# Kernel tuning notes

Measured on AMD Instinct MI355X. Metric: run time of the kernel, lower is better.

The kernel has to match this reference:

```python
import jax, jax.numpy as jnp
import numpy as np

N_SIDE = 32          # dense voxel grid side
WINDOW = 8           # window_size
C = 512              # channels
H = 8                # num_heads
D = C // H           # head_dim = 64
EPS = 1e-12          # torch F.normalize eps


def setup_inputs() -> dict:
    key = jax.random.key(0)
    ks = jax.random.split(key, 4)
    N = N_SIDE ** 3
    g = jnp.arange(N_SIDE, dtype=jnp.int32)
    zz, yy, xx = jnp.meshgrid(g, g, g, indexing='ij')
    # coords: [N, 4] = (batch_idx, x, y, z)
    coords = jnp.stack([jnp.zeros((N,), jnp.int32),
                        xx.reshape(-1), yy.reshape(-1), zz.reshape(-1)], axis=-1)
    x_feats = jax.random.normal(ks[0], (N, C), jnp.float32)
    w_qkv = jax.random.normal(ks[1], (C, 3 * C), jnp.float32) / np.sqrt(C).astype(np.float32)
    b_qkv = jnp.zeros((3 * C,), jnp.float32)
    gamma_q = jnp.ones((H, D), jnp.float32)
    gamma_k = jnp.ones((H, D), jnp.float32)
    w_out = jax.random.normal(ks[2], (C, C), jnp.float32) / np.sqrt(C).astype(np.float32)
    b_out = jnp.zeros((C,), jnp.float32)
    return dict(x_feats=x_feats, coords=coords, w_qkv=w_qkv, b_qkv=b_qkv,
                gamma_q=gamma_q, gamma_k=gamma_k, w_out=w_out, b_out=b_out)


def _mh_rms_norm(x, gamma):
    # SparseMultiHeadRMSNorm: L2-normalize last dim, scale by gamma * sqrt(dim)
    xf = x.astype(jnp.float32)
    norm = jnp.maximum(jnp.linalg.norm(xf, axis=-1, keepdims=True), EPS)
    return ((xf / norm) * gamma * np.float32(np.sqrt(D))).astype(x.dtype)


def reference(x_feats, coords, w_qkv, b_qkv, gamma_q, gamma_k, w_out, b_out):
    N = x_feats.shape[0]
    qkv = (x_feats @ w_qkv + b_qkv).reshape(N, 3, H, D)  # [N,3,H,D]
    q = _mh_rms_norm(qkv[:, 0], gamma_q)
    k = _mh_rms_norm(qkv[:, 1], gamma_k)
    v = qkv[:, 2]
    # windowed grouping: window id from voxel coords (shift_window = (0,0,0))
    wc = coords[:, 1:] // WINDOW                       # [N,3]
    nwin = N_SIDE // WINDOW
    wid = (wc[:, 0] * nwin + wc[:, 1]) * nwin + wc[:, 2]
    order = jnp.argsort(wid, stable=True)              # gather points into windows
    inv = jnp.argsort(order)                           # scatter back
    M = WINDOW ** 3                                    # points per window (dense grid)
    W = N // M                                         # number of windows
    qg = q[order].reshape(W, M, H, D)
    kg = k[order].reshape(W, M, H, D)
    vg = v[order].reshape(W, M, H, D)
    scores = jnp.einsum('wmhd,wnhd->whmn', qg, kg) / np.float32(np.sqrt(D))
    attn = jax.nn.softmax(scores, axis=-1)
    hg = jnp.einsum('whmn,wnhd->wmhd', attn, vg)       # [W,M,H,D]
    h = hg.reshape(W * M, H * D)[inv]                  # back to original point order
    return h @ w_out + b_out
```

## Files before the change

kernel.cpp:

```cpp
#include <hip/hip_runtime.h>


typedef __attribute__((ext_vector_type(4))) float f32x4;
typedef __attribute__((ext_vector_type(8))) short s16x8;

#define MFMA(a, b, c) __builtin_amdgcn_mfma_f32_16x16x32_bf16((a), (b), (c), 0, 0, 0)

__device__ __forceinline__ short f2bf(float f) {
  union { float f; unsigned u; } v; v.f = f;
  unsigned r = v.u + 0x7fffu + ((v.u >> 16) & 1u);
  return (short)(r >> 16);
}

__device__ __forceinline__ void gload16(const void* g, void* l) {
  __builtin_amdgcn_global_load_lds(
      (const __attribute__((address_space(1))) unsigned int*)g,
      (__attribute__((address_space(3))) unsigned int*)l, 16, 0, 0);
}

__global__ __launch_bounds__(256) void transpose_w(const float* __restrict__ w,
                                                   short* __restrict__ wt,
                                                   int Ncols) {
  __shared__ float tile[64][65];
  const int t = threadIdx.x;
  const int ntn = Ncols >> 6;
  const int bk = blockIdx.x / ntn, bn = blockIdx.x % ntn;
  const int c = t & 63, r0 = t >> 6;
#pragma unroll
  for (int i = 0; i < 16; ++i) {
    int k = i * 4 + r0;
    tile[k][c] = w[(size_t)(bk * 64 + k) * Ncols + bn * 64 + c];
  }
  __syncthreads();
#pragma unroll
  for (int i = 0; i < 16; ++i) {
    int n = i * 4 + r0;
    wt[(size_t)(bn * 64 + n) * 512 + bk * 64 + c] = f2bf(tile[c][n]);
  }
}

__global__ __launch_bounds__(256) void gather_x(const float* __restrict__ x,
                                                const int* __restrict__ coords,
                                                short* __restrict__ xs,
                                                int* __restrict__ nofp) {
  const int t = threadIdx.x, lane = t & 63, wid = t >> 6;
  const int n = blockIdx.x * 4 + wid;
  const int cx = coords[n * 4 + 1], cy = coords[n * 4 + 2], cz = coords[n * 4 + 3];
  const int w = ((cx >> 3) * 4 + (cy >> 3)) * 4 + (cz >> 3);
  const int r = ((cz & 7) << 6) | ((cy & 7) << 3) | (cx & 7);
  const int p = w * 512 + r;
  const f32x4* xr = (const f32x4*)(x + (size_t)n * 512);
  f32x4 v0 = xr[lane * 2], v1 = xr[lane * 2 + 1];
  s16x8 o;
  o[0] = f2bf(v0[0]); o[1] = f2bf(v0[1]); o[2] = f2bf(v0[2]); o[3] = f2bf(v0[3]);
  o[4] = f2bf(v1[0]); o[5] = f2bf(v1[1]); o[6] = f2bf(v1[2]); o[7] = f2bf(v1[3]);
  *(s16x8*)(xs + (size_t)p * 512 + lane * 8) = o;
  if (lane == 0) nofp[p] = n;
}

__global__ __launch_bounds__(256) void gemm_qkv(
    const short* __restrict__ xs, const short* __restrict__ wt,
    const float* __restrict__ bqkv, const float* __restrict__ gq,
    const float* __restrict__ gk, short* __restrict__ Qs,
    short* __restrict__ Ks, short* __restrict__ Vt) {
  __shared__ short As[128 * 32];
  __shared__ short Bs[128 * 32];
  const int t = threadIdx.x, lane = t & 63, wid = t >> 6;
  const int bm = blockIdx.x / 12, bn = blockIdx.x % 12;
  const int wr = wid >> 1, wc = wid & 1;
  const int rowbase = bm * 128, colbase = bn * 128;
  f32x4 acc[4][4];
#pragma unroll
  for (int m = 0; m < 4; ++m)
#pragma unroll
    for (int n = 0; n < 4; ++n) acc[m][n] = (f32x4){0.f, 0.f, 0.f, 0.f};

  const int srow = lane >> 2, sslot = lane & 3;
  for (int kt = 0; kt < 16; ++kt) {
#pragma unroll
    for (int i = 0; i < 2; ++i) {
      int row = i * 64 + wid * 16 + srow;
      int gc = sslot ^ ((row >> 2) & 3);
      gload16(xs + (size_t)(rowbase + row) * 512 + kt * 32 + gc * 8,
              &As[(i * 64 + wid * 16) * 32]);
      gload16(wt + (size_t)(colbase + row) * 512 + kt * 32 + gc * 8,
              &Bs[(i * 64 + wid * 16) * 32]);
    }
    __syncthreads();
    s16x8 af[4], bfr[4];
#pragma unroll
    for (int m = 0; m < 4; ++m) {
      int row = wr * 64 + m * 16 + (lane & 15);
      int ch = (lane >> 4) ^ ((row >> 2) & 3);
      af[m] = *(const s16x8*)&As[row * 32 + ch * 8];
    }
#pragma unroll
    for (int n = 0; n < 4; ++n) {
      int row = wc * 64 + n * 16 + (lane & 15);
      int ch = (lane >> 4) ^ ((row >> 2) & 3);
      bfr[n] = *(const s16x8*)&Bs[row * 32 + ch * 8];
    }
#pragma unroll
    for (int m = 0; m < 4; ++m)
#pragma unroll
      for (int n = 0; n < 4; ++n) acc[m][n] = MFMA(af[m], bfr[n], acc[m][n]);
    __syncthreads();
  }

  const int wcb = colbase + wc * 64;
  const int which = wcb >> 9;
  const int h = (wcb >> 6) & 7;
  float bias[4], gam[4];
#pragma unroll
  for (int n = 0; n < 4; ++n) {
    int d = n * 16 + (lane & 15);
    bias[n] = bqkv[wcb + d];
    gam[n] = (which == 0) ? gq[h * 64 + d] : (which == 1) ? gk[h * 64 + d] : 1.0f;
  }
#pragma unroll
  for (int m = 0; m < 4; ++m) {
#pragma unroll
    for (int n = 0; n < 4; ++n)
#pragma unroll
      for (int j = 0; j < 4; ++j) acc[m][n][j] += bias[n];
    float scl[4] = {1.f, 1.f, 1.f, 1.f};
    if (which < 2) {
      float ss[4] = {0.f, 0.f, 0.f, 0.f};
#pragma unroll
      for (int n = 0; n < 4; ++n)
#pragma unroll
        for (int j = 0; j < 4; ++j) ss[j] += acc[m][n][j] * acc[m][n][j];
#pragma unroll
      for (int j = 0; j < 4; ++j) {
#pragma unroll
        for (int msk = 1; msk < 16; msk <<= 1) ss[j] += __shfl_xor(ss[j], msk, 64);
        float nrm = fmaxf(sqrtf(ss[j]), 1e-12f);
        scl[j] = ((which == 0) ? 1.0f : 8.0f) / nrm;
      }
    }
#pragma unroll
    for (int j = 0; j < 4; ++j) {
      int p = rowbase + wr * 64 + m * 16 + (lane >> 4) * 4 + j;
      int w = p >> 9, mm = p & 511;
#pragma unroll
      for (int n = 0; n < 4; ++n) {
        int d = n * 16 + (lane & 15);
        float v = acc[m][n][j];
        if (which == 0)
          Qs[((w * 8 + h) * 512 + mm) * 64 + d] = f2bf(v * gam[n] * scl[j]);
        else if (which == 1)
          Ks[((w * 8 + h) * 512 + mm) * 64 + d] = f2bf(v * gam[n] * scl[j]);
        else
          Vt[((w * 8 + h) * 64 + d) * 512 + mm] = f2bf(v);
      }
    }
  }
}

__global__ __launch_bounds__(256) void attn_k(const short* __restrict__ Qs,
                                              const short* __restrict__ Ks,
                                              const short* __restrict__ Vt,
                                              short* __restrict__ Hs) {
  extern __shared__ short smem[];
  short* Kl = smem;
  short* Vl = smem + 128 * 64;
  short* Pl = smem + 2 * 128 * 64;
  const int t = threadIdx.x, lane = t & 63, wid = t >> 6;
  const int qt = blockIdx.x & 3, wh = blockIdx.x >> 2;
  const short* Qb = Qs + (size_t)wh * 512 * 64;
  const short* Kb = Ks + (size_t)wh * 512 * 64;
  const short* Vb = Vt + (size_t)wh * 64 * 512;

  s16x8 aq[2][2];
#pragma unroll
  for (int m = 0; m < 2; ++m)
#pragma unroll
    for (int ks = 0; ks < 2; ++ks) {
      int row = qt * 128 + wid * 32 + m * 16 + (lane & 15);
      aq[m][ks] = *(const s16x8*)&Qb[row * 64 + ks * 32 + (lane >> 4) * 8];
    }
  f32x4 oacc[2][4];
  float rm[2][4], rl[2][4];
#pragma unroll
  for (int m = 0; m < 2; ++m) {
#pragma unroll
    for (int n = 0; n < 4; ++n) oacc[m][n] = (f32x4){0.f, 0.f, 0.f, 0.f};
#pragma unroll
    for (int j = 0; j < 4; ++j) { rm[m][j] = -1e30f; rl[m][j] = 0.f; }
  }

  for (int kt = 0; kt < 4; ++kt) {
    __syncthreads();
#pragma unroll
    for (int i = 0; i < 4; ++i) {
      int row = i * 32 + wid * 8 + (lane >> 3);
      int gc = (lane & 7) ^ (row & 7);
      gload16(Kb + (size_t)(kt * 128 + row) * 64 + gc * 8,
              &Kl[(i * 32 + wid * 8) * 64]);
    }
#pragma unroll
    for (int i = 0; i < 4; ++i) {
      int dr = i * 16 + wid * 4 + (lane >> 4);
      int gc = (lane & 15) ^ (dr & 15);
      gload16(Vb + (size_t)dr * 512 + kt * 128 + gc * 8,
              &Vl[(i * 16 + wid * 4) * 128]);
    }
    __syncthreads();

    f32x4 s[2][8];
#pragma unroll
    for (int m = 0; m < 2; ++m)
#pragma unroll
      for (int n = 0; n < 8; ++n) s[m][n] = (f32x4){0.f, 0.f, 0.f, 0.f};
#pragma unroll
    for (int ks = 0; ks < 2; ++ks)
#pragma unroll
      for (int n = 0; n < 8; ++n) {
        int kr = n * 16 + (lane & 15);
        int ch = (ks * 4 + (lane >> 4)) ^ (kr & 7);
        s16x8 bk = *(const s16x8*)&Kl[kr * 64 + ch * 8];
        s[0][n] = MFMA(aq[0][ks], bk, s[0][n]);
        s[1][n] = MFMA(aq[1][ks], bk, s[1][n]);
      }

#pragma unroll
    for (int m = 0; m < 2; ++m)
#pragma unroll
      for (int j = 0; j < 4; ++j) {
        float v = s[m][0][j];
#pragma unroll
        for (int n = 1; n < 8; ++n) v = fmaxf(v, s[m][n][j]);
#pragma unroll
        for (int msk = 1; msk < 16; msk <<= 1) v = fmaxf(v, __shfl_xor(v, msk, 64));
        float nm = fmaxf(rm[m][j], v);
        float f = __expf(rm[m][j] - nm);
        rm[m][j] = nm;
        float sum = 0.f;
#pragma unroll
        for (int n = 0; n < 8; ++n) {
          float pe = __expf(s[m][n][j] - nm);
          s[m][n][j] = pe;
          sum += pe;
        }
#pragma unroll
        for (int msk = 1; msk < 16; msk <<= 1) sum += __shfl_xor(sum, msk, 64);
        rl[m][j] = rl[m][j] * f + sum;
#pragma unroll
        for (int n2 = 0; n2 < 4; ++n2) oacc[m][n2][j] *= f;
      }

#pragma unroll
    for (int m = 0; m < 2; ++m)
#pragma unroll
      for (int n = 0; n < 8; ++n)
#pragma unroll
        for (int j = 0; j < 4; ++j) {
          int row = wid * 32 + m * 16 + (lane >> 4) * 4 + j;
          int col = n * 16 + (lane & 15);
          int ch = (col >> 3) ^ (row & 15);
          Pl[row * 128 + ch * 8 + (col & 7)] = f2bf(s[m][n][j]);
        }

#pragma unroll
    for (int ks = 0; ks < 4; ++ks) {
      s16x8 ap[2];
#pragma unroll
      for (int m = 0; m < 2; ++m) {
        int row = wid * 32 + m * 16 + (lane & 15);
        int ch = (ks * 4 + (lane >> 4)) ^ (row & 15);
        ap[m] = *(const s16x8*)&Pl[row * 128 + ch * 8];
      }
#pragma unroll
      for (int n2 = 0; n2 < 4; ++n2) {
        int dr = n2 * 16 + (lane & 15);
        int ch = (ks * 4 + (lane >> 4)) ^ (dr & 15);
        s16x8 bv = *(const s16x8*)&Vl[dr * 128 + ch * 8];
        oacc[0][n2] = MFMA(ap[0], bv, oacc[0][n2]);
        oacc[1][n2] = MFMA(ap[1], bv, oacc[1][n2]);
      }
    }
  }

  const int w = wh >> 3, hh = wh & 7;
#pragma unroll
  for (int m = 0; m < 2; ++m)
#pragma unroll
    for (int j = 0; j < 4; ++j) {
      float inv = 1.0f / rl[m][j];
      int row = qt * 128 + wid * 32 + m * 16 + (lane >> 4) * 4 + j;
      int p = w * 512 + row;
#pragma unroll
      for (int n2 = 0; n2 < 4; ++n2) {
        int d = n2 * 16 + (lane & 15);
        Hs[(size_t)p * 512 + hh * 64 + d] = f2bf(oacc[m][n2][j] * inv);
      }
    }
}

__global__ __launch_bounds__(256) void gemm_out_k(
    const short* __restrict__ Hs, const short* __restrict__ wt,
    const float* __restrict__ bout, const int* __restrict__ nofp,
    float* __restrict__ out) {
  __shared__ short As[128 * 32];
  __shared__ short Bs[128 * 32];
  const int t = threadIdx.x, lane = t & 63, wid = t >> 6;
  const int bm = blockIdx.x >> 2, bn = blockIdx.x & 3;
  const int wr = wid >> 1, wc = wid & 1;
  const int rowbase = bm * 128, colbase = bn * 128;
  f32x4 acc[4][4];
#pragma unroll
  for (int m = 0; m < 4; ++m)
#pragma unroll
    for (int n = 0; n < 4; ++n) acc[m][n] = (f32x4){0.f, 0.f, 0.f, 0.f};

  const int srow = lane >> 2, sslot = lane & 3;
  for (int kt = 0; kt < 16; ++kt) {
#pragma unroll
    for (int i = 0; i < 2; ++i) {
      int row = i * 64 + wid * 16 + srow;
      int gc = sslot ^ ((row >> 2) & 3);
      gload16(Hs + (size_t)(rowbase + row) * 512 + kt * 32 + gc * 8,
              &As[(i * 64 + wid * 16) * 32]);
      gload16(wt + (size_t)(colbase + row) * 512 + kt * 32 + gc * 8,
              &Bs[(i * 64 + wid * 16) * 32]);
    }
    __syncthreads();
    s16x8 af[4], bfr[4];
#pragma unroll
    for (int m = 0; m < 4; ++m) {
      int row = wr * 64 + m * 16 + (lane & 15);
      int ch = (lane >> 4) ^ ((row >> 2) & 3);
      af[m] = *(const s16x8*)&As[row * 32 + ch * 8];
    }
#pragma unroll
    for (int n = 0; n < 4; ++n) {
      int row = wc * 64 + n * 16 + (lane & 15);
      int ch = (lane >> 4) ^ ((row >> 2) & 3);
      bfr[n] = *(const s16x8*)&Bs[row * 32 + ch * 8];
    }
#pragma unroll
    for (int m = 0; m < 4; ++m)
#pragma unroll
      for (int n = 0; n < 4; ++n) acc[m][n] = MFMA(af[m], bfr[n], acc[m][n]);
    __syncthreads();
  }
#pragma unroll
  for (int m = 0; m < 4; ++m)
#pragma unroll
    for (int j = 0; j < 4; ++j) {
      int p = rowbase + wr * 64 + m * 16 + (lane >> 4) * 4 + j;
      int norig = nofp[p];
#pragma unroll
      for (int n = 0; n < 4; ++n) {
        int c = colbase + wc * 64 + n * 16 + (lane & 15);
        out[(size_t)norig * 512 + c] = acc[m][n][j] + bout[c];
      }
    }
}

extern "C" void kernel_launch(void* const* d_in, const int* in_sizes, int n_in,
                              void* d_out, int out_size, void* d_ws,
                              size_t ws_size, hipStream_t stream) {
  const float* x      = (const float*)d_in[0];
  const int*   coords = (const int*)d_in[1];
  const float* wqkv   = (const float*)d_in[2];
  const float* bqkv   = (const float*)d_in[3];
  const float* gq     = (const float*)d_in[4];
  const float* gk     = (const float*)d_in[5];
  const float* wout   = (const float*)d_in[6];
  const float* bout   = (const float*)d_in[7];
  float* out = (float*)d_out;
  char* ws = (char*)d_ws;

  short* xs    = (short*)(ws + 0);
  short* wqkvt = (short*)(ws + 33554432);
  short* woutt = (short*)(ws + 35127296);
  short* Qs    = (short*)(ws + 35651584);
  short* Ks    = (short*)(ws + 69206016);
  short* Vt    = (short*)(ws + 102760448);
  short* Hs    = (short*)(ws + 136314880);
  int*   nofp  = (int*)(ws + 169869312);

  transpose_w<<<dim3(192), dim3(256), 0, stream>>>(wqkv, wqkvt, 1536);
  transpose_w<<<dim3(64), dim3(256), 0, stream>>>(wout, woutt, 512);
  gather_x<<<dim3(8192), dim3(256), 0, stream>>>(x, coords, xs, nofp);
  gemm_qkv<<<dim3(3072), dim3(256), 0, stream>>>(xs, wqkvt, bqkv, gq, gk, Qs, Ks, Vt);
  attn_k<<<dim3(2048), dim3(256), 65536, stream>>>(Qs, Ks, Vt, Hs);
  gemm_out_k<<<dim3(1024), dim3(256), 0, stream>>>(Hs, woutt, bout, nofp, out);
}
```

Measured before the change: 425.2 us.

## Restructure attention into per-wave query tiles reading K/V directly from global

```diff
diff --git a/kernel.cpp b/kernel.cpp
--- a/kernel.cpp
+++ b/kernel.cpp
@@ -3,6 +3,7 @@
 
 typedef __attribute__((ext_vector_type(4))) float f32x4;
 typedef __attribute__((ext_vector_type(8))) short s16x8;
+typedef __attribute__((ext_vector_type(4))) short s16x4;
 
 #define MFMA(a, b, c) __builtin_amdgcn_mfma_f32_16x16x32_bf16((a), (b), (c), 0, 0, 0)
 
@@ -123,13 +124,13 @@
     for (int n = 0; n < 4; ++n)
 #pragma unroll
       for (int j = 0; j < 4; ++j) acc[m][n][j] += bias[n];
-    float scl[4] = {1.f, 1.f, 1.f, 1.f};
     if (which < 2) {
       float ss[4] = {0.f, 0.f, 0.f, 0.f};
 #pragma unroll
       for (int n = 0; n < 4; ++n)
 #pragma unroll
         for (int j = 0; j < 4; ++j) ss[j] += acc[m][n][j] * acc[m][n][j];
+      float scl[4];
 #pragma unroll
       for (int j = 0; j < 4; ++j) {
 #pragma unroll
@@ -137,21 +138,30 @@
         float nrm = fmaxf(sqrtf(ss[j]), 1e-12f);
         scl[j] = ((which == 0) ? 1.0f : 8.0f) / nrm;
       }
-    }
-#pragma unroll
-    for (int j = 0; j < 4; ++j) {
-      int p = rowbase + wr * 64 + m * 16 + (lane >> 4) * 4 + j;
-      int w = p >> 9, mm = p & 511;
+#pragma unroll
+      for (int j = 0; j < 4; ++j) {
+        int p = rowbase + wr * 64 + m * 16 + (lane >> 4) * 4 + j;
+        int w = p >> 9, mm = p & 511;
+#pragma unroll
+        for (int n = 0; n < 4; ++n) {
+          int d = n * 16 + (lane & 15);
+          float v = acc[m][n][j] * gam[n] * scl[j];
+          if (which == 0)
+            Qs[((w * 8 + h) * 512 + mm) * 64 + d] = f2bf(v);
+          else
+            Ks[((w * 8 + h) * 512 + mm) * 64 + d] = f2bf(v);
+        }
+      }
+    } else {
+      int pb = rowbase + wr * 64 + m * 16 + (lane >> 4) * 4;
+      int w = pb >> 9, mm = pb & 511;
 #pragma unroll
       for (int n = 0; n < 4; ++n) {
         int d = n * 16 + (lane & 15);
-        float v = acc[m][n][j];
-        if (which == 0)
-          Qs[((w * 8 + h) * 512 + mm) * 64 + d] = f2bf(v * gam[n] * scl[j]);
-        else if (which == 1)
-          Ks[((w * 8 + h) * 512 + mm) * 64 + d] = f2bf(v * gam[n] * scl[j]);
-        else
-          Vt[((w * 8 + h) * 64 + d) * 512 + mm] = f2bf(v);
+        s16x4 pk;
+#pragma unroll
+        for (int j = 0; j < 4; ++j) pk[j] = f2bf(acc[m][n][j]);
+        *(s16x4*)&Vt[((size_t)(w * 8 + h) * 64 + d) * 512 + mm] = pk;
       }
     }
   }
@@ -161,120 +171,106 @@
                                               const short* __restrict__ Ks,
                                               const short* __restrict__ Vt,
                                               short* __restrict__ Hs) {
-  extern __shared__ short smem[];
-  short* Kl = smem;
-  short* Vl = smem + 128 * 64;
-  short* Pl = smem + 2 * 128 * 64;
+  __shared__ short Pl[4][32 * 64];
   const int t = threadIdx.x, lane = t & 63, wid = t >> 6;
-  const int qt = blockIdx.x & 3, wh = blockIdx.x >> 2;
+  const int bid = blockIdx.x;
+  const int swz = (bid & 7) * 256 + (bid >> 3);
+  const int wv = swz * 4 + wid;
+  const int wh = wv >> 4;
+  const int qt = wv & 15;
   const short* Qb = Qs + (size_t)wh * 512 * 64;
   const short* Kb = Ks + (size_t)wh * 512 * 64;
   const short* Vb = Vt + (size_t)wh * 64 * 512;
+  short* slab = Pl[wid];
 
   s16x8 aq[2][2];
 #pragma unroll
-  for (int m = 0; m < 2; ++m)
+  for (int mi = 0; mi < 2; ++mi)
 #pragma unroll
     for (int ks = 0; ks < 2; ++ks) {
-      int row = qt * 128 + wid * 32 + m * 16 + (lane & 15);
-      aq[m][ks] = *(const s16x8*)&Qb[row * 64 + ks * 32 + (lane >> 4) * 8];
+      int row = qt * 32 + mi * 16 + (lane & 15);
+      aq[mi][ks] = *(const s16x8*)&Qb[row * 64 + ks * 32 + (lane >> 4) * 8];
     }
   f32x4 oacc[2][4];
   float rm[2][4], rl[2][4];
 #pragma unroll
-  for (int m = 0; m < 2; ++m) {
-#pragma unroll
-    for (int n = 0; n < 4; ++n) oacc[m][n] = (f32x4){0.f, 0.f, 0.f, 0.f};
-#pragma unroll
-    for (int j = 0; j < 4; ++j) { rm[m][j] = -1e30f; rl[m][j] = 0.f; }
-  }
-
-  for (int kt = 0; kt < 4; ++kt) {
-    __syncthreads();
-#pragma unroll
-    for (int i = 0; i < 4; ++i) {
-      int row = i * 32 + wid * 8 + (lane >> 3);
-      int gc = (lane & 7) ^ (row & 7);
-      gload16(Kb + (size_t)(kt * 128 + row) * 64 + gc * 8,
-              &Kl[(i * 32 + wid * 8) * 64]);
-    }
-#pragma unroll
-    for (int i = 0; i < 4; ++i) {
-      int dr = i * 16 + wid * 4 + (lane >> 4);
-      int gc = (lane & 15) ^ (dr & 15);
-      gload16(Vb + (size_t)dr * 512 + kt * 128 + gc * 8,
-              &Vl[(i * 16 + wid * 4) * 128]);
-    }
-    __syncthreads();
-
-    f32x4 s[2][8];
-#pragma unroll
-    for (int m = 0; m < 2; ++m)
-#pragma unroll
-      for (int n = 0; n < 8; ++n) s[m][n] = (f32x4){0.f, 0.f, 0.f, 0.f};
+  for (int mi = 0; mi < 2; ++mi) {
+#pragma unroll
+    for (int n = 0; n < 4; ++n) oacc[mi][n] = (f32x4){0.f, 0.f, 0.f, 0.f};
+#pragma unroll
+    for (int j = 0; j < 4; ++j) { rm[mi][j] = -1e30f; rl[mi][j] = 0.f; }
+  }
+
+  for (int kt = 0; kt < 8; ++kt) {
+    const int kb = kt * 64;
+    f32x4 s[2][4];
+#pragma unroll
+    for (int mi = 0; mi < 2; ++mi)
+#pragma unroll
+      for (int n = 0; n < 4; ++n) s[mi][n] = (f32x4){0.f, 0.f, 0.f, 0.f};
 #pragma unroll
     for (int ks = 0; ks < 2; ++ks)
 #pragma unroll
-      for (int n = 0; n < 8; ++n) {
-        int kr = n * 16 + (lane & 15);
-        int ch = (ks * 4 + (lane >> 4)) ^ (kr & 7);
-        s16x8 bk = *(const s16x8*)&Kl[kr * 64 + ch * 8];
+      for (int n = 0; n < 4; ++n) {
+        int kr = kb + n * 16 + (lane & 15);
+        s16x8 bk = *(const s16x8*)&Kb[kr * 64 + ks * 32 + (lane >> 4) * 8];
         s[0][n] = MFMA(aq[0][ks], bk, s[0][n]);
         s[1][n] = MFMA(aq[1][ks], bk, s[1][n]);
       }
 
 #pragma unroll
-    for (int m = 0; m < 2; ++m)
+    for (int mi = 0; mi < 2; ++mi)
 #pragma unroll
       for (int j = 0; j < 4; ++j) {
-        float v = s[m][0][j];
-#pragma unroll
-        for (int n = 1; n < 8; ++n) v = fmaxf(v, s[m][n][j]);
+        float v = fmaxf(fmaxf(s[mi][0][j], s[mi][1][j]),
+                        fmaxf(s[mi][2][j], s[mi][3][j]));
 #pragma unroll
         for (int msk = 1; msk < 16; msk <<= 1) v = fmaxf(v, __shfl_xor(v, msk, 64));
-        float nm = fmaxf(rm[m][j], v);
-        float f = __expf(rm[m][j] - nm);
-        rm[m][j] = nm;
+        if (!__all(v - rm[mi][j] <= 8.0f)) {
+          float nm = fmaxf(rm[mi][j], v);
+          float f = __expf(rm[mi][j] - nm);
+          rm[mi][j] = nm;
+          rl[mi][j] *= f;
+#pragma unroll
+          for (int n2 = 0; n2 < 4; ++n2) oacc[mi][n2][j] *= f;
+        }
         float sum = 0.f;
 #pragma unroll
-        for (int n = 0; n < 8; ++n) {
-          float pe = __expf(s[m][n][j] - nm);
-          s[m][n][j] = pe;
+        for (int n = 0; n < 4; ++n) {
+          float pe = __expf(s[mi][n][j] - rm[mi][j]);
+          s[mi][n][j] = pe;
           sum += pe;
         }
 #pragma unroll
         for (int msk = 1; msk < 16; msk <<= 1) sum += __shfl_xor(sum, msk, 64);
-        rl[m][j] = rl[m][j] * f + sum;
-#pragma unroll
-        for (int n2 = 0; n2 < 4; ++n2) oacc[m][n2][j] *= f;
-      }
-
-#pragma unroll
-    for (int m = 0; m < 2; ++m)
-#pragma unroll
-      for (int n = 0; n < 8; ++n)
+        rl[mi][j] += sum;
+      }
+
+#pragma unroll
+    for (int mi = 0; mi < 2; ++mi)
+#pragma unroll
+      for (int n = 0; n < 4; ++n)
 #pragma unroll
         for (int j = 0; j < 4; ++j) {
-          int row = wid * 32 + m * 16 + (lane >> 4) * 4 + j;
+          int r = mi * 16 + (lane >> 4) * 4 + j;
           int col = n * 16 + (lane & 15);
-          int ch = (col >> 3) ^ (row & 15);
-          Pl[row * 128 + ch * 8 + (col & 7)] = f2bf(s[m][n][j]);
+          slab[r * 64 + (((col >> 3) ^ (r & 7)) << 3) + (col & 7)] =
+              f2bf(s[mi][n][j]);
         }
 
 #pragma unroll
-    for (int ks = 0; ks < 4; ++ks) {
+    for (int ks = 0; ks < 2; ++ks) {
       s16x8 ap[2];
 #pragma unroll
-      for (int m = 0; m < 2; ++m) {
-        int row = wid * 32 + m * 16 + (lane & 15);
-        int ch = (ks * 4 + (lane >> 4)) ^ (row & 15);
-        ap[m] = *(const s16x8*)&Pl[row * 128 + ch * 8];
+      for (int mi = 0; mi < 2; ++mi) {
+        int row = mi * 16 + (lane & 15);
+        int ch = (ks * 4 + (lane >> 4)) ^ (row & 7);
+        ap[mi] = *(const s16x8*)&slab[row * 64 + ch * 8];
       }
 #pragma unroll
       for (int n2 = 0; n2 < 4; ++n2) {
         int dr = n2 * 16 + (lane & 15);
-        int ch = (ks * 4 + (lane >> 4)) ^ (dr & 15);
-        s16x8 bv = *(const s16x8*)&Vl[dr * 128 + ch * 8];
+        s16x8 bv = *(const s16x8*)&Vb[dr * 512 + kb + ks * 32 + (lane >> 4) * 8];
         oacc[0][n2] = MFMA(ap[0], bv, oacc[0][n2]);
         oacc[1][n2] = MFMA(ap[1], bv, oacc[1][n2]);
       }
@@ -283,16 +279,16 @@
 
   const int w = wh >> 3, hh = wh & 7;
 #pragma unroll
-  for (int m = 0; m < 2; ++m)
+  for (int mi = 0; mi < 2; ++mi)
 #pragma unroll
     for (int j = 0; j < 4; ++j) {
-      float inv = 1.0f / rl[m][j];
-      int row = qt * 128 + wid * 32 + m * 16 + (lane >> 4) * 4 + j;
+      float inv = 1.0f / rl[mi][j];
+      int row = qt * 32 + mi * 16 + (lane >> 4) * 4 + j;
       int p = w * 512 + row;
 #pragma unroll
       for (int n2 = 0; n2 < 4; ++n2) {
         int d = n2 * 16 + (lane & 15);
-        Hs[(size_t)p * 512 + hh * 64 + d] = f2bf(oacc[m][n2][j] * inv);
+        Hs[(size_t)p * 512 + hh * 64 + d] = f2bf(oacc[mi][n2][j] * inv);
       }
     }
 }
@@ -385,6 +381,6 @@
   transpose_w<<<dim3(64), dim3(256), 0, stream>>>(wout, woutt, 512);
   gather_x<<<dim3(8192), dim3(256), 0, stream>>>(x, coords, xs, nofp);
   gemm_qkv<<<dim3(3072), dim3(256), 0, stream>>>(xs, wqkvt, bqkv, gq, gk, Qs, Ks, Vt);
-  attn_k<<<dim3(2048), dim3(256), 65536, stream>>>(Qs, Ks, Vt, Hs);
+  attn_k<<<dim3(2048), dim3(256), 0, stream>>>(Qs, Ks, Vt, Hs);
   gemm_out_k<<<dim3(1024), dim3(256), 0, stream>>>(Hs, woutt, bout, nofp, out);
 }
```

Result: no change. 427.4 us (+0.5%).
